# Kernel tuning notes

Hardware: AMD Instinct MI355X
Metric: run time of the kernel (lower is better)

The kernel has to match this reference:

```python
import jax, jax.numpy as jnp
import numpy as np

S = 60            # voxel grid side
N = 100000        # active voxels
M_PAD = 60000     # padded pairs per kernel offset
C_IN = 64
C_OUT = 64
KV = 27           # kernel volume (3^3)
CENTER = 13


def _build_maps():
    rng = np.random.default_rng(0)
    lin = rng.choice(S ** 3, size=N, replace=False)
    coords = np.stack(np.unravel_index(lin, (S, S, S)), axis=1).astype(np.int64)  # [N,3]
    lut = -np.ones(S ** 3, dtype=np.int64)
    lut[lin] = np.arange(N)
    imap = -np.ones((KV - 1, M_PAD), dtype=np.int32)
    omap = -np.ones((KV - 1, M_PAD), dtype=np.int32)
    row = 0
    for k in range(KV):
        if k == CENTER:
            continue
        d = np.array([k // 9 - 1, (k // 3) % 3 - 1, k % 3 - 1])
        nb = coords + d
        valid = np.all((nb >= 0) & (nb < S), axis=1)
        linnb = nb[:, 0] * S * S + nb[:, 1] * S + nb[:, 2]
        j = np.where(valid, lut[np.clip(linnb, 0, S ** 3 - 1)], -1)
        mask = j >= 0
        src = np.nonzero(mask)[0].astype(np.int32)   # input idx (gather)
        dst = j[mask].astype(np.int32)               # output idx (scatter)
        m = min(src.shape[0], M_PAD)
        imap[row, :m] = src[:m]
        omap[row, :m] = dst[:m]
        row += 1
    return imap, omap


def setup_inputs() -> dict:
    key = jax.random.key(0)
    kf, kw = jax.random.split(key)
    feats = jax.random.normal(kf, (N, C_IN), dtype=jnp.float32)
    stdv = 1.0 / np.sqrt(C_OUT * KV)
    kernel = jax.random.uniform(kw, (KV, C_IN, C_OUT), dtype=jnp.float32,
                                minval=-stdv, maxval=stdv)
    imap_np, omap_np = _build_maps()
    return {
        "feats": feats,
        "kernel": kernel,
        "imap": jnp.asarray(imap_np),
        "omap": jnp.asarray(omap_np),
    }


def reference(feats, kernel, imap, omap):
    # Submanifold sparse 3D conv: center weight applied densely,
    # 26 neighbor offsets via gather -> per-offset GEMM -> scatter-add.
    # feats: [N, Cin], kernel: [27, Cin, Cout], imap/omap: [26, M] (-1 = pad)
    koff = jnp.concatenate([jnp.arange(CENTER), jnp.arange(CENTER + 1, KV)])
    w_off = kernel[koff]                                   # [26, Cin, Cout]
    out = feats @ kernel[CENTER]                           # [N, Cout] center GEMM
    valid = (imap >= 0)                                    # [26, M]
    gathered = feats[jnp.clip(imap, 0)] * valid[..., None].astype(feats.dtype)  # [26, M, Cin]
    partial = jnp.einsum('kmc,kco->kmo', gathered, w_off)  # [26, M, Cout]
    dst = jnp.where(valid, omap, 0).reshape(-1)            # padded rows contribute zeros
    out = out.at[dst].add(partial.reshape(-1, partial.shape[-1]))
    return out
```

## Files before the change

kernel.cpp:

```cpp
#include <hip/hip_runtime.h>


#define N_PTS 100000
#define MPAD  60000
#define C     64
#define NSL   27

typedef short bf16x8 __attribute__((ext_vector_type(8)));
typedef float f32x4  __attribute__((ext_vector_type(4)));

static __device__ inline unsigned short f2bf(float x) {
    unsigned int u = __float_as_uint(x);
    u += 0x7fffu + ((u >> 16) & 1u);
    return (unsigned short)(u >> 16);
}

#define FEATS16_BYTES ((size_t)(N_PTS + 1) * C * 2)
#define WFRAG_OFF     (((FEATS16_BYTES) + 255) & ~(size_t)255)
#define WFRAG_BYTES   ((size_t)NSL * 2 * 4 * 64 * 16)
#define NBR_OFF       (WFRAG_OFF + WFRAG_BYTES)
#define NBR_BYTES     ((size_t)26 * N_PTS * 4)

__global__ __launch_bounds__(256) void prep_feats(const float* __restrict__ feats,
                                                  unsigned short* __restrict__ f16) {
    const int idx = blockIdx.x * 256 + threadIdx.x;
    const int total = (N_PTS * C) / 8;
    bf16x8* dst = (bf16x8*)f16;
    if (idx < total) {
        const float4* src = (const float4*)feats;
        const float4 a = src[2 * idx];
        const float4 b = src[2 * idx + 1];
        bf16x8 v;
        v[0] = (short)f2bf(a.x); v[1] = (short)f2bf(a.y);
        v[2] = (short)f2bf(a.z); v[3] = (short)f2bf(a.w);
        v[4] = (short)f2bf(b.x); v[5] = (short)f2bf(b.y);
        v[6] = (short)f2bf(b.z); v[7] = (short)f2bf(b.w);
        dst[idx] = v;
    } else if (idx < total + 8) {
        bf16x8 z = (bf16x8){0, 0, 0, 0, 0, 0, 0, 0};
        dst[idx] = z;
    }
}

__global__ __launch_bounds__(256) void prep_wfrag(const float* __restrict__ kern,
                                                  unsigned short* __restrict__ wf) {
    const int idx = blockIdx.x * 256 + threadIdx.x;
    if (idx >= NSL * 2 * 4 * 64) return;
    const int lane = idx & 63;
    const int rest = idx >> 6;
    const int ct = rest & 3;
    const int kk = (rest >> 2) & 1;
    const int s  = rest >> 3;
    const int q = lane >> 4, t = lane & 15;
    const int ksrc = (s == 26) ? 13 : (s + (s >= 13 ? 1 : 0));
    const int k0 = kk * 32 + q * 8;
    const int n  = ct * 16 + t;
    const float* w = kern + (size_t)ksrc * 4096 + n;
    bf16x8 v;
    #pragma unroll
    for (int j = 0; j < 8; ++j) v[j] = (short)f2bf(w[(size_t)(k0 + j) * 64]);
    ((bf16x8*)wf)[idx] = v;
}

__global__ __launch_bounds__(256) void prep_nbr(const int* __restrict__ imap,
                                                const int* __restrict__ omap,
                                                int* __restrict__ nbr) {
    const int m = blockIdx.x * 256 + threadIdx.x;
    const int s = blockIdx.y;
    if (m < MPAD) {
        const int i = imap[(size_t)s * MPAD + m];
        if (i >= 0) nbr[(size_t)s * N_PTS + omap[(size_t)s * MPAD + m]] = i;
    }
}

__global__ __launch_bounds__(256) void spconv_main(const unsigned short* __restrict__ f16,
                                                   const unsigned short* __restrict__ wf,
                                                   const int* __restrict__ nbr,
                                                   float* __restrict__ out) {
    const int lane = threadIdx.x & 63;
    const int wave = threadIdx.x >> 6;
    const int q = lane >> 4, t = lane & 15;
    const int R0 = blockIdx.x * 128 + wave * 32;

    f32x4 acc[2][4];
    #pragma unroll
    for (int a = 0; a < 2; ++a)
        #pragma unroll
        for (int c = 0; c < 4; ++c)
            acc[a][c] = (f32x4){0.f, 0.f, 0.f, 0.f};

    const bf16x8* wfv = (const bf16x8*)wf;

    for (int s = 0; s < NSL; ++s) {
        bf16x8 B[2][4];
        #pragma unroll
        for (int kk = 0; kk < 2; ++kk)
            #pragma unroll
            for (int ct = 0; ct < 4; ++ct)
                B[kk][ct] = wfv[s * 512 + kk * 256 + ct * 64 + lane];

        #pragma unroll
        for (int tile = 0; tile < 2; ++tile) {
            const int row = R0 + tile * 16 + t;
            int j = -1;
            if (row < N_PTS)
                j = (s == 26) ? row : nbr[(size_t)s * N_PTS + row];
            if (!__any(j >= 0)) continue;
            const int jz = (j >= 0) ? j : N_PTS;
            const bf16x8* ar = (const bf16x8*)(f16 + (size_t)jz * C);
            const bf16x8 A0 = ar[q];
            const bf16x8 A1 = ar[4 + q];
            #pragma unroll
            for (int ct = 0; ct < 4; ++ct)
                acc[tile][ct] = __builtin_amdgcn_mfma_f32_16x16x32_bf16(A0, B[0][ct], acc[tile][ct], 0, 0, 0);
            #pragma unroll
            for (int ct = 0; ct < 4; ++ct)
                acc[tile][ct] = __builtin_amdgcn_mfma_f32_16x16x32_bf16(A1, B[1][ct], acc[tile][ct], 0, 0, 0);
        }
    }

    #pragma unroll
    for (int tile = 0; tile < 2; ++tile) {
        #pragma unroll
        for (int i = 0; i < 4; ++i) {
            const int row = R0 + tile * 16 + 4 * q + i;
            if (row < N_PTS) {
                #pragma unroll
                for (int ct = 0; ct < 4; ++ct)
                    out[(size_t)row * C + ct * 16 + t] = acc[tile][ct][i];
            }
        }
    }
}

extern "C" void kernel_launch(void* const* d_in, const int* in_sizes, int n_in,
                              void* d_out, int out_size, void* d_ws, size_t ws_size,
                              hipStream_t stream) {
    const float* feats = (const float*)d_in[0];
    const float* kern  = (const float*)d_in[1];
    const int*   imap  = (const int*)d_in[2];
    const int*   omap  = (const int*)d_in[3];

    char* ws = (char*)d_ws;
    unsigned short* f16 = (unsigned short*)ws;
    unsigned short* wf  = (unsigned short*)(ws + WFRAG_OFF);
    int*            nbr = (int*)(ws + NBR_OFF);

    hipMemsetAsync(nbr, 0xFF, NBR_BYTES, stream);

    prep_feats<<<dim3((800008 + 255) / 256), dim3(256), 0, stream>>>(feats, f16);
    prep_wfrag<<<dim3((NSL * 2 * 4 * 64 + 255) / 256), dim3(256), 0, stream>>>(kern, wf);
    prep_nbr<<<dim3((MPAD + 255) / 256, 26), dim3(256), 0, stream>>>(imap, omap, nbr);

    spconv_main<<<dim3((N_PTS + 127) / 128), dim3(256), 0, stream>>>(
        f16, wf, nbr, (float*)d_out);
}
```

Measured before the change: 167.4 us.

## Fuse prep kernels and software-pipeline neighbor gathers in sparse conv

Merges the memset, feature conversion and weight-fragment prep into one kernel, and vectorizes the neighbor-map scatter to int4 loads. The main kernel is fully unrolled over the 27 offsets and prefetches neighbor indices two steps ahead and gathered feature rows one step ahead, so global-load latency overlaps with MFMA work. It also drops the per-tile skip of empty offsets and interleaves the two tiles' MFMAs. The large unrolled arrays raise register pressure, which can cut occupancy.

```diff
diff --git a/kernel.cpp b/kernel.cpp
--- a/kernel.cpp
+++ b/kernel.cpp
@@ -21,56 +21,67 @@
 #define NBR_OFF       (WFRAG_OFF + WFRAG_BYTES)
 #define NBR_BYTES     ((size_t)26 * N_PTS * 4)
 
-__global__ __launch_bounds__(256) void prep_feats(const float* __restrict__ feats,
-                                                  unsigned short* __restrict__ f16) {
+#define FEAT_ITEMS 800008
+#define WF_ITEMS   (NSL * 2 * 4 * 64)
+#define NBRF_ITEMS (26 * N_PTS / 4)
+#define PREP_TOTAL (FEAT_ITEMS + WF_ITEMS + NBRF_ITEMS)
+
+__global__ __launch_bounds__(256) void prep_all(const float* __restrict__ feats,
+                                                const float* __restrict__ kern,
+                                                unsigned short* __restrict__ f16,
+                                                unsigned short* __restrict__ wf,
+                                                int* __restrict__ nbr) {
     const int idx = blockIdx.x * 256 + threadIdx.x;
-    const int total = (N_PTS * C) / 8;
-    bf16x8* dst = (bf16x8*)f16;
-    if (idx < total) {
-        const float4* src = (const float4*)feats;
-        const float4 a = src[2 * idx];
-        const float4 b = src[2 * idx + 1];
+    if (idx < FEAT_ITEMS) {
+        bf16x8* dst = (bf16x8*)f16;
+        if (idx < FEAT_ITEMS - 8) {
+            const float4* src = (const float4*)feats;
+            const float4 a = src[2 * idx];
+            const float4 b = src[2 * idx + 1];
+            bf16x8 v;
+            v[0] = (short)f2bf(a.x); v[1] = (short)f2bf(a.y);
+            v[2] = (short)f2bf(a.z); v[3] = (short)f2bf(a.w);
+            v[4] = (short)f2bf(b.x); v[5] = (short)f2bf(b.y);
+            v[6] = (short)f2bf(b.z); v[7] = (short)f2bf(b.w);
+            dst[idx] = v;
+        } else {
+            dst[idx] = (bf16x8){0, 0, 0, 0, 0, 0, 0, 0};
+        }
+    } else if (idx < FEAT_ITEMS + WF_ITEMS) {
+        const int w = idx - FEAT_ITEMS;
+        const int lane = w & 63;
+        const int rest = w >> 6;
+        const int ct = rest & 3;
+        const int kk = (rest >> 2) & 1;
+        const int s  = rest >> 3;
+        const int q = lane >> 4, t = lane & 15;
+        const int ksrc = (s == 26) ? 13 : (s + (s >= 13 ? 1 : 0));
+        const int k0 = kk * 32 + q * 8;
+        const int n  = ct * 16 + t;
+        const float* wp = kern + (size_t)ksrc * 4096 + n;
         bf16x8 v;
-        v[0] = (short)f2bf(a.x); v[1] = (short)f2bf(a.y);
-        v[2] = (short)f2bf(a.z); v[3] = (short)f2bf(a.w);
-        v[4] = (short)f2bf(b.x); v[5] = (short)f2bf(b.y);
-        v[6] = (short)f2bf(b.z); v[7] = (short)f2bf(b.w);
-        dst[idx] = v;
-    } else if (idx < total + 8) {
-        bf16x8 z = (bf16x8){0, 0, 0, 0, 0, 0, 0, 0};
-        dst[idx] = z;
+        #pragma unroll
+        for (int j = 0; j < 8; ++j) v[j] = (short)f2bf(wp[(size_t)(k0 + j) * 64]);
+        ((bf16x8*)wf)[w] = v;
+    } else {
+        const int k = idx - (FEAT_ITEMS + WF_ITEMS);
+        if (k < NBRF_ITEMS) ((int4*)nbr)[k] = make_int4(-1, -1, -1, -1);
     }
-}
-
-__global__ __launch_bounds__(256) void prep_wfrag(const float* __restrict__ kern,
-                                                  unsigned short* __restrict__ wf) {
-    const int idx = blockIdx.x * 256 + threadIdx.x;
-    if (idx >= NSL * 2 * 4 * 64) return;
-    const int lane = idx & 63;
-    const int rest = idx >> 6;
-    const int ct = rest & 3;
-    const int kk = (rest >> 2) & 1;
-    const int s  = rest >> 3;
-    const int q = lane >> 4, t = lane & 15;
-    const int ksrc = (s == 26) ? 13 : (s + (s >= 13 ? 1 : 0));
-    const int k0 = kk * 32 + q * 8;
-    const int n  = ct * 16 + t;
-    const float* w = kern + (size_t)ksrc * 4096 + n;
-    bf16x8 v;
-    #pragma unroll
-    for (int j = 0; j < 8; ++j) v[j] = (short)f2bf(w[(size_t)(k0 + j) * 64]);
-    ((bf16x8*)wf)[idx] = v;
 }
 
 __global__ __launch_bounds__(256) void prep_nbr(const int* __restrict__ imap,
                                                 const int* __restrict__ omap,
                                                 int* __restrict__ nbr) {
-    const int m = blockIdx.x * 256 + threadIdx.x;
+    const int v = blockIdx.x * 256 + threadIdx.x;
     const int s = blockIdx.y;
-    if (m < MPAD) {
-        const int i = imap[(size_t)s * MPAD + m];
-        if (i >= 0) nbr[(size_t)s * N_PTS + omap[(size_t)s * MPAD + m]] = i;
-    }
+    if (v >= MPAD / 4) return;
+    const int4 iv = ((const int4*)(imap + (size_t)s * MPAD))[v];
+    const int4 ov = ((const int4*)(omap + (size_t)s * MPAD))[v];
+    int* nb = nbr + (size_t)s * N_PTS;
+    if (iv.x >= 0) nb[ov.x] = iv.x;
+    if (iv.y >= 0) nb[ov.y] = iv.y;
+    if (iv.z >= 0) nb[ov.z] = iv.z;
+    if (iv.w >= 0) nb[ov.w] = iv.w;
 }
 
 __global__ __launch_bounds__(256) void spconv_main(const unsigned short* __restrict__ f16,
@@ -81,6 +92,21 @@
     const int wave = threadIdx.x >> 6;
     const int q = lane >> 4, t = lane & 15;
     const int R0 = blockIdx.x * 128 + wave * 32;
+    const int row0 = R0 + t;
+    const int row1 = R0 + 16 + t;
+
+    const bf16x8* wfv = (const bf16x8*)wf;
+    const bf16x8* fv  = (const bf16x8*)f16;
+
+    auto ldj = [&](int s, int row) -> int {
+        if (s == 26) return (row < N_PTS) ? row : -1;
+        const int rc = (row < N_PTS) ? row : 0;
+        const int j = nbr[(size_t)s * N_PTS + rc];
+        return (row < N_PTS) ? j : -1;
+    };
+    auto clampj = [&](int j) -> int {
+        return ((unsigned)j < (unsigned)N_PTS) ? j : N_PTS;
+    };
 
     f32x4 acc[2][4];
     #pragma unroll
@@ -89,33 +115,45 @@
         for (int c = 0; c < 4; ++c)
             acc[a][c] = (f32x4){0.f, 0.f, 0.f, 0.f};
 
-    const bf16x8* wfv = (const bf16x8*)wf;
+    int j0[NSL], j1[NSL];
+    bf16x8 A[NSL][4];
 
+    j0[0] = ldj(0, row0); j1[0] = ldj(0, row1);
+    j0[1] = ldj(1, row0); j1[1] = ldj(1, row1);
+    {
+        const bf16x8* a0 = fv + (size_t)clampj(j0[0]) * 8;
+        const bf16x8* a1 = fv + (size_t)clampj(j1[0]) * 8;
+        A[0][0] = a0[q]; A[0][1] = a0[4 + q];
+        A[0][2] = a1[q]; A[0][3] = a1[4 + q];
+    }
+
+    #pragma unroll
     for (int s = 0; s < NSL; ++s) {
-        bf16x8 B[2][4];
+        if (s + 2 < NSL) {
+            j0[s + 2] = ldj(s + 2, row0);
+            j1[s + 2] = ldj(s + 2, row1);
+        }
+        if (s + 1 < NSL) {
+            const bf16x8* a0 = fv + (size_t)clampj(j0[s + 1]) * 8;
+            const bf16x8* a1 = fv + (size_t)clampj(j1[s + 1]) * 8;
+            A[s + 1][0] = a0[q]; A[s + 1][1] = a0[4 + q];
+            A[s + 1][2] = a1[q]; A[s + 1][3] = a1[4 + q];
+        }
+        bf16x8 B0[4], B1[4];
         #pragma unroll
-        for (int kk = 0; kk < 2; ++kk)
-            #pragma unroll
-            for (int ct = 0; ct < 4; ++ct)
-                B[kk][ct] = wfv[s * 512 + kk * 256 + ct * 64 + lane];
-
+        for (int ct = 0; ct < 4; ++ct) {
+            B0[ct] = wfv[s * 512 + ct * 64 + lane];
+            B1[ct] = wfv[s * 512 + 256 + ct * 64 + lane];
+        }
         #pragma unroll
-        for (int tile = 0; tile < 2; ++tile) {
-            const int row = R0 + tile * 16 + t;
-            int j = -1;
-            if (row < N_PTS)
-                j = (s == 26) ? row : nbr[(size_t)s * N_PTS + row];
-            if (!__any(j >= 0)) continue;
-            const int jz = (j >= 0) ? j : N_PTS;
-            const bf16x8* ar = (const bf16x8*)(f16 + (size_t)jz * C);
-            const bf16x8 A0 = ar[q];
-            const bf16x8 A1 = ar[4 + q];
-            #pragma unroll
-            for (int ct = 0; ct < 4; ++ct)
-                acc[tile][ct] = __builtin_amdgcn_mfma_f32_16x16x32_bf16(A0, B[0][ct], acc[tile][ct], 0, 0, 0);
-            #pragma unroll
-            for (int ct = 0; ct < 4; ++ct)
-                acc[tile][ct] = __builtin_amdgcn_mfma_f32_16x16x32_bf16(A1, B[1][ct], acc[tile][ct], 0, 0, 0);
+        for (int ct = 0; ct < 4; ++ct) {
+            acc[0][ct] = __builtin_amdgcn_mfma_f32_16x16x32_bf16(A[s][0], B0[ct], acc[0][ct], 0, 0, 0);
+            acc[1][ct] = __builtin_amdgcn_mfma_f32_16x16x32_bf16(A[s][2], B0[ct], acc[1][ct], 0, 0, 0);
+        }
+        #pragma unroll
+        for (int ct = 0; ct < 4; ++ct) {
+            acc[0][ct] = __builtin_amdgcn_mfma_f32_16x16x32_bf16(A[s][1], B1[ct], acc[0][ct], 0, 0, 0);
+            acc[1][ct] = __builtin_amdgcn_mfma_f32_16x16x32_bf16(A[s][3], B1[ct], acc[1][ct], 0, 0, 0);
         }
     }
 
@@ -146,12 +184,10 @@
     unsigned short* wf  = (unsigned short*)(ws + WFRAG_OFF);
     int*            nbr = (int*)(ws + NBR_OFF);
 
-    hipMemsetAsync(nbr, 0xFF, NBR_BYTES, stream);
-
-    prep_feats<<<dim3((800008 + 255) / 256), dim3(256), 0, stream>>>(feats, f16);
-    prep_wfrag<<<dim3((NSL * 2 * 4 * 64 + 255) / 256), dim3(256), 0, stream>>>(kern, wf);
-    prep_nbr<<<dim3((MPAD + 255) / 256, 26), dim3(256), 0, stream>>>(imap, omap, nbr);
-
+    prep_all<<<dim3((PREP_TOTAL + 255) / 256), dim3(256), 0, stream>>>(
+        feats, kern, f16, wf, nbr);
+    prep_nbr<<<dim3((MPAD / 4 + 255) / 256, 26), dim3(256), 0, stream>>>(
+        imap, omap, nbr);
     spconv_main<<<dim3((N_PTS + 127) / 128), dim3(256), 0, stream>>>(
         f16, wf, nbr, (float*)d_out);
 }
```

New measurement: 166.9 us. Within noise of the previous version (-0.3%).
